# Performance work log

Hardware: AMD Instinct MI355X
Metric: run time of the kernel (lower is better)

Reference implementation:

```python
import jax, jax.numpy as jnp
import numpy as np

B, S, H = 2, 1024, 2048
NH, NKV, HD = 32, 8, 64          # head_dim = H // NH
G = NH // NKV                    # GQA group size = 4
THETA = 500000.0
EPS = 1e-5
SCALE = HD ** -0.5


def _rope_neox(x, positions):
    # x: [B, S, n_heads, HD]; neox style: rotate concatenated halves
    inv_freq = 1.0 / (THETA ** (jnp.arange(0, HD, 2, dtype=jnp.float32) / HD))  # [HD/2]
    ang = positions[..., None].astype(jnp.float32) * inv_freq                    # [B, S, HD/2]
    cos = jnp.cos(ang)[:, :, None, :]
    sin = jnp.sin(ang)[:, :, None, :]
    x1, x2 = jnp.split(x, 2, axis=-1)
    return jnp.concatenate([x1 * cos - x2 * sin, x2 * cos + x1 * sin], axis=-1)


def setup_inputs() -> dict:
    key = jax.random.key(0)
    k1, k2, k3 = jax.random.split(key, 3)
    hidden_states = jax.random.normal(k1, (B, S, H), jnp.float32)
    w_qkv = jax.random.normal(k2, ((NH + 2 * NKV) * HD, H), jnp.float32) * 0.02
    w_o = jax.random.normal(k3, (H, NH * HD), jnp.float32) * 0.02
    norm_w = jnp.ones((H,), jnp.float32)
    positions = jnp.broadcast_to(jnp.arange(S, dtype=jnp.int32), (B, S))
    return {"hidden_states": hidden_states, "positions": positions,
            "w_qkv": w_qkv, "w_o": w_o, "norm_w": norm_w}


def reference(hidden_states, positions, w_qkv, w_o, norm_w):
    # QKV projection (bias=False) and split
    qkv = hidden_states @ w_qkv.T                                 # [B,S,3072]
    q, k, v = jnp.split(qkv, [NH * HD, NH * HD + NKV * HD], axis=-1)
    q = q.reshape(B, S, NH, HD)
    k = k.reshape(B, S, NKV, HD)
    v = v.reshape(B, S, NKV, HD)

    # RoPE on q and k (full rotary_dim = head_dim)
    q = _rope_neox(q, positions)
    k = _rope_neox(k, positions)

    # Causal GQA attention (dense-prefill equivalent of RadixAttention)
    qg = q.reshape(B, S, NKV, G, HD)
    scores = jnp.einsum('bqhgd,bkhd->bhgqk', qg, k) * SCALE       # [B,NKV,G,S,S]
    causal = jnp.tril(jnp.ones((S, S), dtype=bool))
    scores = jnp.where(causal, scores, jnp.float32(-1e30))
    probs = jax.nn.softmax(scores, axis=-1)
    attn = jnp.einsum('bhgqk,bkhd->bqhgd', probs, v).reshape(B, S, NH * HD)

    # BitNet sub-norm (RMSNorm) then output projection
    var = jnp.mean(attn * attn, axis=-1, keepdims=True)
    normed = attn * jax.lax.rsqrt(var + EPS) * norm_w
    return normed @ w_o.T                                         # [B,S,H]
```

## Files before the change

### kernel.cpp

```cpp
#include <hip/hip_runtime.h>
#include <hip/hip_bf16.h>
#include <cstdint>
#include <cstddef>

typedef __bf16 bf16;
typedef __bf16 bf16x2 __attribute__((ext_vector_type(2)));
typedef __bf16 bf16x4 __attribute__((ext_vector_type(4)));
typedef __bf16 bf16x8 __attribute__((ext_vector_type(8)));
typedef float  f32x4  __attribute__((ext_vector_type(4)));

__device__ __forceinline__ void async_copy16(const void* g, void* l) {
  __builtin_amdgcn_global_load_lds((const __attribute__((address_space(1))) void*)g,
                                   (__attribute__((address_space(3))) void*)l,
                                   16, 0, 0);
}

__device__ __forceinline__ bool block_flag_is_f32(const unsigned int* w, int tid,
                                                  int* sflag) {
  if (tid < 64) {
    int weird = 0;
#pragma unroll
    for (int c = 0; c < 2; ++c) {
      const unsigned int lo = w[c * 64 + tid] & 0xffffu;
      const unsigned int ex = (lo >> 7) & 0xffu;
      if (ex >= 134u) ++weird;
    }
    const unsigned long long m1 = __ballot(weird >= 1);
    const unsigned long long m2 = __ballot(weird == 2);
    if (tid == 0) *sflag = (__popcll(m1) + __popcll(m2) >= 8) ? 1 : 0;
  }
  __syncthreads();
  return *sflag != 0;
}

__global__ __launch_bounds__(256) void convert_all(
    const void* __restrict__ s0, const void* __restrict__ s1,
    const void* __restrict__ s2, const void* __restrict__ s3,
    bf16* __restrict__ d0, bf16* __restrict__ d1, bf16* __restrict__ d2,
    float* __restrict__ ssum) {
  __shared__ int sflag;
  const int tid = threadIdx.x;
  const bool f32 = block_flag_is_f32((const unsigned int*)s0, tid, &sflag);
  if (blockIdx.x == 0) {
    ((float4*)ssum)[tid * 2]     = make_float4(0.f, 0.f, 0.f, 0.f);
    ((float4*)ssum)[tid * 2 + 1] = make_float4(0.f, 0.f, 0.f, 0.f);
  }
  const int i = blockIdx.x * 256 + tid;
  if (i >= 3670016) return;
  const void* src; bf16* dst; int off; bool fold = false;
  if      (i < 1048576) { src = s0; dst = d0; off = i; }
  else if (i < 2621440) { src = s1; dst = d1; off = i - 1048576; }
  else                  { src = s2; dst = d2; off = i - 2621440; fold = true; }
  float v[4];
  if (f32) {
    const float4 t = ((const float4*)src)[off];
    v[0] = t.x; v[1] = t.y; v[2] = t.z; v[3] = t.w;
  } else {
    const bf16x4 t = ((const bf16x4*)src)[off];
#pragma unroll
    for (int j = 0; j < 4; ++j) v[j] = (float)t[j];
  }
  if (fold) {
    const int k0 = (off * 4) & 2047;
#pragma unroll
    for (int j = 0; j < 4; ++j) {
      const float w = f32 ? ((const float*)s3)[k0 + j] : (float)((const bf16*)s3)[k0 + j];
      v[j] *= w;
    }
  }
  bf16x4 o;
#pragma unroll
  for (int j = 0; j < 4; ++j) o[j] = (bf16)v[j];
  *(bf16x4*)(dst + (size_t)off * 4) = o;
}

__global__ __launch_bounds__(256) void gemm_qkv_rope(
    const bf16* __restrict__ A, const bf16* __restrict__ B,
    const int* __restrict__ pos,
    bf16* __restrict__ Q, bf16* __restrict__ K, bf16* __restrict__ V)
{
  __shared__ __align__(16) bf16 As[4 * 64 * 32];
  __shared__ __align__(16) bf16 Bs[4 * 128 * 32];
  const int tid = threadIdx.x, wave = tid >> 6, lane = tid & 63;
  const int l15 = lane & 15, l4 = lane >> 4;
  const int m0 = blockIdx.y * 64, n0 = blockIdx.x * 128;
  const int wm = (wave >> 1) * 32, wn = (wave & 1) * 64;
  const int KD = 2048;

  f32x4 acc[2][4] = {};

  for (int kt = 0; kt < KD; kt += 128) {
#pragma unroll
    for (int c = 0; c < 4; ++c) {
      const int e = c * 2048 + tid * 8;
      const int kc = e >> 11, row = (e >> 5) & 63, o = e & 31;
      async_copy16(A + (size_t)(m0 + row) * KD + kt + kc * 32 + o, As + e);
    }
#pragma unroll
    for (int c = 0; c < 8; ++c) {
      const int e = c * 2048 + tid * 8;
      const int kc = e >> 12, row = (e >> 5) & 127, o = e & 31;
      async_copy16(B + (size_t)(n0 + row) * KD + kt + kc * 32 + o, Bs + e);
    }
    __syncthreads();
#pragma unroll
    for (int s = 0; s < 4; ++s) {
      bf16x8 af[2], bfr[4];
#pragma unroll
      for (int i = 0; i < 2; ++i)
        af[i] = *(const bf16x8*)(As + s * 2048 + (wm + i * 16 + l15) * 32 + l4 * 8);
#pragma unroll
      for (int j = 0; j < 4; ++j)
        bfr[j] = *(const bf16x8*)(Bs + s * 4096 + (wn + j * 16 + l15) * 32 + l4 * 8);
#pragma unroll
      for (int i = 0; i < 2; ++i)
#pragma unroll
        for (int j = 0; j < 4; ++j)
          acc[i][j] = __builtin_amdgcn_mfma_f32_16x16x32_bf16(af[i], bfr[j], acc[i][j], 0, 0, 0);
    }
    __syncthreads();
  }

  if (n0 < 2560) {
    const bool isQ = (n0 < 2048);
#pragma unroll
    for (int i = 0; i < 2; ++i)
#pragma unroll
      for (int j = 0; j < 4; ++j) {
        const int col = n0 + wn + j * 16 + l15;
        const int hd = isQ ? col : (col - 2048);
        const int hh = hd >> 6, d = hd & 63;
        const int fi = d & 31;
        const float ifr = __expf((float)fi * -0.41007385554f);
#pragma unroll
        for (int r = 0; r < 4; ++r) {
          const int m = m0 + wm + i * 16 + l4 * 4 + r;
          const int b = m >> 10, s = m & 1023;
          const float ang = (float)pos[m] * ifr;
          float sn, cs;
          __sincosf(ang, &sn, &cs);
          const float x  = acc[i][j][r];
          const float xp = acc[i][j ^ 2][r];
          const float v = (d < 32) ? (x * cs - xp * sn) : (x * cs + xp * sn);
          if (isQ) Q[(((size_t)(b * 32 + hh)) * 1024 + s) * 64 + d] = (bf16)(v * 0.125f);
          else     K[(((size_t)(b * 8 + hh)) * 1024 + s) * 64 + d] = (bf16)v;
        }
      }
  } else {
#pragma unroll
    for (int i = 0; i < 2; ++i)
#pragma unroll
      for (int j = 0; j < 4; ++j) {
        const int cv = n0 + wn + j * 16 + l15 - 2560;
        const int hh = cv >> 6, d = cv & 63;
#pragma unroll
        for (int r = 0; r < 4; ++r) {
          const int m = m0 + wm + i * 16 + l4 * 4 + r;
          const int b = m >> 10, s = m & 1023;
          const int sp = (s & ~31) + ((s & 15) * 2 + ((s >> 4) & 1));
          V[(((size_t)(b * 8 + hh)) * 64 + d) * 1024 + sp] = (bf16)acc[i][j][r];
        }
      }
  }
}

__global__ __launch_bounds__(256) void attn_kernel(
    const bf16* __restrict__ Q, const bf16* __restrict__ K,
    const bf16* __restrict__ Vt, bf16* __restrict__ O, float* __restrict__ ssum)
{
  __shared__ __align__(16) bf16 Ks[2 * 128 * 32];
  __shared__ __align__(16) bf16 Vs[4 * 64 * 32];
  __shared__ __align__(16) bf16 Ps[4 * 128 * 40];

  const int tid = threadIdx.x, wave = tid >> 6, lane = tid & 63;
  const int l15 = lane & 15, l4 = lane >> 4;
  const int ip = blockIdx.x, bh = blockIdx.y;
  const int b = bh >> 5, h = bh & 31, kvh = h >> 2;
  const int qlo = ip * 64, qhi = (15 - ip) * 64;
  const bf16* Qb = Q + ((size_t)(b * 32 + h)) * 65536;
  const bf16* Kb = K + ((size_t)(b * 8 + kvh)) * 65536;
  const bf16* Vb = Vt + ((size_t)(b * 8 + kvh)) * 65536;

#pragma unroll
  for (int c = 0; c < 4; ++c) {
    const int e = c * 2048 + tid * 8;
    const int dchunk = e >> 12;
    const int row = (e & 4095) >> 5;
    const int qb = (row < 64) ? qlo : qhi;
    async_copy16(Qb + (size_t)(qb + (row & 63)) * 64 + dchunk * 32 + (e & 31), Ps + e);
  }
  __syncthreads();
  bf16x8 aq[2][2];
#pragma unroll
  for (int i = 0; i < 2; ++i)
#pragma unroll
    for (int s = 0; s < 2; ++s)
      aq[i][s] = *(const bf16x8*)(Ps + s * 4096 + (i * 64 + wave * 16 + l15) * 32 + l4 * 8);
  __syncthreads();

  float m_s[2][4], l_s[2][4];
  f32x4 o_acc[2][4] = {};
#pragma unroll
  for (int i = 0; i < 2; ++i)
#pragma unroll
    for (int r = 0; r < 4; ++r) { m_s[i][r] = -3.0e4f; l_s[i][r] = 0.f; }

  const int nkt = (1151 - 64 * ip) >> 7;
  for (int kt = 0; kt < nkt; ++kt) {
    const int k0 = kt * 128;
    const bool lo_act = (k0 < (ip + 1) * 64);
#pragma unroll
    for (int c = 0; c < 4; ++c) {
      const int e = c * 2048 + tid * 8;
      const int dchunk = e >> 12;
      const int krow = (e & 4095) >> 5;
      async_copy16(Kb + (size_t)(k0 + krow) * 64 + dchunk * 32 + (e & 31), Ks + e);
      const int kc = e >> 11;
      const int drow = (e & 2047) >> 5;
      async_copy16(Vb + (size_t)drow * 1024 + k0 + kc * 32 + (e & 31), Vs + e);
    }
    __syncthreads();

    f32x4 sc[2][8] = {};
#pragma unroll
    for (int j = 0; j < 8; ++j) {
      const bf16x8 bk0 = *(const bf16x8*)(Ks + (j * 16 + l15) * 32 + l4 * 8);
      const bf16x8 bk1 = *(const bf16x8*)(Ks + 4096 + (j * 16 + l15) * 32 + l4 * 8);
      sc[1][j] = __builtin_amdgcn_mfma_f32_16x16x32_bf16(aq[1][0], bk0, sc[1][j], 0, 0, 0);
      sc[1][j] = __builtin_amdgcn_mfma_f32_16x16x32_bf16(aq[1][1], bk1, sc[1][j], 0, 0, 0);
      if (lo_act) {
        sc[0][j] = __builtin_amdgcn_mfma_f32_16x16x32_bf16(aq[0][0], bk0, sc[0][j], 0, 0, 0);
        sc[0][j] = __builtin_amdgcn_mfma_f32_16x16x32_bf16(aq[0][1], bk1, sc[0][j], 0, 0, 0);
      }
    }

#pragma unroll
    for (int hh = 0; hh < 2; ++hh) {
      if (hh == 0 && !lo_act) continue;
      const int qb = hh ? qhi : qlo;
#pragma unroll
      for (int r = 0; r < 4; ++r) {
        const int rl = wave * 16 + l4 * 4 + r;
        const int rg = qb + rl;
        float mx = -3.0e4f;
#pragma unroll
        for (int j = 0; j < 8; ++j) {
          float v = sc[hh][j][r];
          if (k0 + j * 16 + l15 > rg) v = -3.0e4f;
          sc[hh][j][r] = v;
          mx = fmaxf(mx, v);
        }
#pragma unroll
        for (int off = 1; off < 16; off <<= 1) mx = fmaxf(mx, __shfl_xor(mx, off));
        const float mnew = fmaxf(m_s[hh][r], mx);
        const float alpha = __expf(m_s[hh][r] - mnew);
        m_s[hh][r] = mnew;
        float rs = 0.f;
#pragma unroll
        for (int t = 0; t < 4; ++t) {
          const float pv0 = __expf(sc[hh][2 * t][r]     - mnew);
          const float pv1 = __expf(sc[hh][2 * t + 1][r] - mnew);
          rs += pv0 + pv1;
          bf16x2 pk; pk[0] = (bf16)pv0; pk[1] = (bf16)pv1;
          *(bf16x2*)(Ps + t * 5120 + (hh * 64 + rl) * 40 + l15 * 2) = pk;
        }
#pragma unroll
        for (int off = 1; off < 16; off <<= 1) rs += __shfl_xor(rs, off);
        l_s[hh][r] = l_s[hh][r] * alpha + rs;
#pragma unroll
        for (int jd = 0; jd < 4; ++jd) o_acc[hh][jd][r] *= alpha;
      }
    }

#pragma unroll
    for (int ks = 0; ks < 4; ++ks) {
      bf16x8 bv[4];
#pragma unroll
      for (int jd = 0; jd < 4; ++jd)
        bv[jd] = *(const bf16x8*)(Vs + ks * 2048 + (jd * 16 + l15) * 32 + l4 * 8);
#pragma unroll
      for (int hh = 0; hh < 2; ++hh) {
        if (hh == 0 && !lo_act) continue;
        const bf16x8 ap = *(const bf16x8*)(Ps + ks * 5120 + (hh * 64 + wave * 16 + l15) * 40 + l4 * 8);
#pragma unroll
        for (int jd = 0; jd < 4; ++jd)
          o_acc[hh][jd] = __builtin_amdgcn_mfma_f32_16x16x32_bf16(ap, bv[jd], o_acc[hh][jd], 0, 0, 0);
      }
    }
    __syncthreads();
  }

#pragma unroll
  for (int hh = 0; hh < 2; ++hh) {
    const int qb = hh ? qhi : qlo;
#pragma unroll
    for (int r = 0; r < 4; ++r) {
      const float inv = 1.0f / l_s[hh][r];
      const int srow = qb + wave * 16 + l4 * 4 + r;
      bf16* op = O + ((size_t)(b * 1024 + srow)) * 2048 + h * 64;
      float ss = 0.f;
#pragma unroll
      for (int jd = 0; jd < 4; ++jd) {
        const float v = o_acc[hh][jd][r] * inv;
        op[jd * 16 + l15] = (bf16)v;
        ss += v * v;
      }
#pragma unroll
      for (int off = 1; off < 16; off <<= 1) ss += __shfl_xor(ss, off);
      if (l15 == 0) atomicAdd(&ssum[b * 1024 + srow], ss);
    }
  }
}

__global__ __launch_bounds__(256) void gemm_out(
    const bf16* __restrict__ A, const bf16* __restrict__ B,
    const float* __restrict__ ssum, const unsigned int* __restrict__ hs_raw,
    void* __restrict__ out)
{
  __shared__ __align__(16) bf16 As[4 * 64 * 32];
  __shared__ __align__(16) bf16 Bs[4 * 128 * 32];
  __shared__ int sflag;
  const int tid = threadIdx.x, wave = tid >> 6, lane = tid & 63;
  const bool f32out = block_flag_is_f32(hs_raw, tid, &sflag);
  const int l15 = lane & 15, l4 = lane >> 4;
  const int m0 = blockIdx.y * 64, n0 = blockIdx.x * 128;
  const int wm = (wave >> 1) * 32, wn = (wave & 1) * 64;
  const int KD = 2048;

  f32x4 acc[2][4] = {};

  for (int kt = 0; kt < KD; kt += 128) {
#pragma unroll
    for (int c = 0; c < 4; ++c) {
      const int e = c * 2048 + tid * 8;
      const int kc = e >> 11, row = (e >> 5) & 63, o = e & 31;
      async_copy16(A + (size_t)(m0 + row) * KD + kt + kc * 32 + o, As + e);
    }
#pragma unroll
    for (int c = 0; c < 8; ++c) {
      const int e = c * 2048 + tid * 8;
      const int kc = e >> 12, row = (e >> 5) & 127, o = e & 31;
      async_copy16(B + (size_t)(n0 + row) * KD + kt + kc * 32 + o, Bs + e);
    }
    __syncthreads();
#pragma unroll
    for (int s = 0; s < 4; ++s) {
      bf16x8 af[2], bfr[4];
#pragma unroll
      for (int i = 0; i < 2; ++i)
        af[i] = *(const bf16x8*)(As + s * 2048 + (wm + i * 16 + l15) * 32 + l4 * 8);
#pragma unroll
      for (int j = 0; j < 4; ++j)
        bfr[j] = *(const bf16x8*)(Bs + s * 4096 + (wn + j * 16 + l15) * 32 + l4 * 8);
#pragma unroll
      for (int i = 0; i < 2; ++i)
#pragma unroll
        for (int j = 0; j < 4; ++j)
          acc[i][j] = __builtin_amdgcn_mfma_f32_16x16x32_bf16(af[i], bfr[j], acc[i][j], 0, 0, 0);
    }
    __syncthreads();
  }

#pragma unroll
  for (int i = 0; i < 2; ++i)
#pragma unroll
    for (int r = 0; r < 4; ++r) {
      const int row = m0 + wm + i * 16 + l4 * 4 + r;
      const float ri = rsqrtf(ssum[row] * (1.0f / 2048.0f) + 1e-5f);
#pragma unroll
      for (int j = 0; j < 4; ++j) {
        const int col = n0 + wn + j * 16 + l15;
        const size_t idx = (size_t)row * 2048 + col;
        const float v = ri * acc[i][j][r];
        if (f32out) ((float*)out)[idx] = v;
        else        ((bf16*)out)[idx]  = (bf16)v;
      }
    }
}

extern "C" void kernel_launch(void* const* d_in, const int* in_sizes, int n_in,
                              void* d_out, int out_size, void* d_ws, size_t ws_size,
                              hipStream_t stream) {
  const void* hs     = d_in[0];
  const int*  pos    = (const int*)d_in[1];
  const void* w_qkv  = d_in[2];
  const void* w_o    = d_in[3];
  const void* norm_w = d_in[4];

  char* ws = (char*)d_ws;
  bf16*  hs_b   = (bf16*) (ws);
  bf16*  wqkv_b = (bf16*) (ws + 8388608);
  bf16*  w_o_b  = (bf16*) (ws + 20971520);
  float* ssum   = (float*)(ws + 29360128);
  bf16*  Qr     = (bf16*) (ws + 29368320);
  bf16*  Kr     = (bf16*) (ws + 37756928);
  bf16*  Vtr    = (bf16*) (ws + 39854080);
  bf16*  attn_o = (bf16*) (ws + 41951232);

  convert_all<<<14336, 256, 0, stream>>>(hs, w_qkv, w_o, norm_w,
                                         hs_b, wqkv_b, w_o_b, ssum);
  gemm_qkv_rope<<<dim3(24, 32), 256, 0, stream>>>(hs_b, wqkv_b, pos, Qr, Kr, Vtr);
  attn_kernel<<<dim3(8, 64), 256, 0, stream>>>(Qr, Kr, Vtr, attn_o, ssum);
  gemm_out<<<dim3(16, 32), 256, 0, stream>>>(attn_o, w_o_b, ssum,
                                             (const unsigned int*)hs, d_out);
}
```

Before: 207.2 us.

## Double-buffer GEMM tiles, swizzle LDS, prefetch K/V via registers, lazy softmax rescale

Both GEMMs now double-buffer 64-wide K tiles, so the next tile's async loads overlap the MFMA work on the current one. LDS layouts gain an XOR swizzle to cut bank conflicts. The attention kernel prefetches the next K/V tile into registers while computing, moves softmax to exp2 by folding log2(e) into the Q scale, and skips the rescale when the running max has not grown by more than 8. The trade-offs are higher register pressure and an extra barrier per attention iteration. The lazy-rescale threshold also lets probabilities exceed 1 before normalization, which costs some bf16 precision in P.

```diff
diff --git a/kernel.cpp b/kernel.cpp
--- a/kernel.cpp
+++ b/kernel.cpp
@@ -14,6 +14,8 @@
                                    (__attribute__((address_space(3))) void*)l,
                                    16, 0, 0);
 }
+
+__device__ __forceinline__ int swz(int row) { return ((row >> 1) & 3) << 3; }
 
 __device__ __forceinline__ bool block_flag_is_f32(const unsigned int* w, int tid,
                                                   int* sflag) {
@@ -79,39 +81,47 @@
     const int* __restrict__ pos,
     bf16* __restrict__ Q, bf16* __restrict__ K, bf16* __restrict__ V)
 {
-  __shared__ __align__(16) bf16 As[4 * 64 * 32];
-  __shared__ __align__(16) bf16 Bs[4 * 128 * 32];
+  __shared__ __align__(16) bf16 As[2][2 * 64 * 32];
+  __shared__ __align__(16) bf16 Bs[2][2 * 128 * 32];
   const int tid = threadIdx.x, wave = tid >> 6, lane = tid & 63;
   const int l15 = lane & 15, l4 = lane >> 4;
   const int m0 = blockIdx.y * 64, n0 = blockIdx.x * 128;
   const int wm = (wave >> 1) * 32, wn = (wave & 1) * 64;
-  const int KD = 2048;
+  const int swz_ro = (l4 * 8) ^ swz(l15);
 
   f32x4 acc[2][4] = {};
 
-  for (int kt = 0; kt < KD; kt += 128) {
+  auto stage = [&](int buf, int kt) {
+#pragma unroll
+    for (int c = 0; c < 2; ++c) {
+      const int e = c * 2048 + tid * 8;
+      const int kc = e >> 11, row = (e >> 5) & 63;
+      const int o = (e & 31) ^ swz(row);
+      async_copy16(A + (size_t)(m0 + row) * 2048 + kt + kc * 32 + o, &As[buf][e]);
+    }
 #pragma unroll
     for (int c = 0; c < 4; ++c) {
       const int e = c * 2048 + tid * 8;
-      const int kc = e >> 11, row = (e >> 5) & 63, o = e & 31;
-      async_copy16(A + (size_t)(m0 + row) * KD + kt + kc * 32 + o, As + e);
-    }
-#pragma unroll
-    for (int c = 0; c < 8; ++c) {
-      const int e = c * 2048 + tid * 8;
-      const int kc = e >> 12, row = (e >> 5) & 127, o = e & 31;
-      async_copy16(B + (size_t)(n0 + row) * KD + kt + kc * 32 + o, Bs + e);
-    }
-    __syncthreads();
-#pragma unroll
-    for (int s = 0; s < 4; ++s) {
+      const int kc = e >> 12, row = (e >> 5) & 127;
+      const int o = (e & 31) ^ swz(row);
+      async_copy16(B + (size_t)(n0 + row) * 2048 + kt + kc * 32 + o, &Bs[buf][e]);
+    }
+  };
+
+  stage(0, 0);
+  __syncthreads();
+  int cur = 0;
+  for (int kt = 0; kt < 2048; kt += 64) {
+    if (kt + 64 < 2048) stage(cur ^ 1, kt + 64);
+#pragma unroll
+    for (int s = 0; s < 2; ++s) {
       bf16x8 af[2], bfr[4];
 #pragma unroll
       for (int i = 0; i < 2; ++i)
-        af[i] = *(const bf16x8*)(As + s * 2048 + (wm + i * 16 + l15) * 32 + l4 * 8);
+        af[i] = *(const bf16x8*)(&As[cur][s * 2048 + (wm + i * 16 + l15) * 32 + swz_ro]);
 #pragma unroll
       for (int j = 0; j < 4; ++j)
-        bfr[j] = *(const bf16x8*)(Bs + s * 4096 + (wn + j * 16 + l15) * 32 + l4 * 8);
+        bfr[j] = *(const bf16x8*)(&Bs[cur][s * 4096 + (wn + j * 16 + l15) * 32 + swz_ro]);
 #pragma unroll
       for (int i = 0; i < 2; ++i)
 #pragma unroll
@@ -119,6 +129,7 @@
           acc[i][j] = __builtin_amdgcn_mfma_f32_16x16x32_bf16(af[i], bfr[j], acc[i][j], 0, 0, 0);
     }
     __syncthreads();
+    cur ^= 1;
   }
 
   if (n0 < 2560) {
@@ -142,7 +153,7 @@
           const float x  = acc[i][j][r];
           const float xp = acc[i][j ^ 2][r];
           const float v = (d < 32) ? (x * cs - xp * sn) : (x * cs + xp * sn);
-          if (isQ) Q[(((size_t)(b * 32 + hh)) * 1024 + s) * 64 + d] = (bf16)(v * 0.125f);
+          if (isQ) Q[(((size_t)(b * 32 + hh)) * 1024 + s) * 64 + d] = (bf16)(v * 0.1803368801f);
           else     K[(((size_t)(b * 8 + hh)) * 1024 + s) * 64 + d] = (bf16)v;
         }
       }
@@ -174,6 +185,7 @@
 
   const int tid = threadIdx.x, wave = tid >> 6, lane = tid & 63;
   const int l15 = lane & 15, l4 = lane >> 4;
+  const int swz_ro = (l4 * 8) ^ swz(l15);
   const int ip = blockIdx.x, bh = blockIdx.y;
   const int b = bh >> 5, h = bh & 31, kvh = h >> 2;
   const int qlo = ip * 64, qhi = (15 - ip) * 64;
@@ -187,7 +199,15 @@
     const int dchunk = e >> 12;
     const int row = (e & 4095) >> 5;
     const int qb = (row < 64) ? qlo : qhi;
-    async_copy16(Qb + (size_t)(qb + (row & 63)) * 64 + dchunk * 32 + (e & 31), Ps + e);
+    const int o = (e & 31) ^ swz(row);
+    async_copy16(Qb + (size_t)(qb + (row & 63)) * 64 + dchunk * 32 + o, Ps + e);
+  }
+  bf16x8 kreg[4], vreg[4];
+#pragma unroll
+  for (int c = 0; c < 4; ++c) {
+    const int e = c * 2048 + tid * 8;
+    kreg[c] = *(const bf16x8*)(Kb + (size_t)((e & 4095) >> 5) * 64 + (e >> 12) * 32 + (e & 31));
+    vreg[c] = *(const bf16x8*)(Vb + (size_t)((e & 2047) >> 5) * 1024 + (e >> 11) * 32 + (e & 31));
   }
   __syncthreads();
   bf16x8 aq[2][2];
@@ -195,7 +215,15 @@
   for (int i = 0; i < 2; ++i)
 #pragma unroll
     for (int s = 0; s < 2; ++s)
-      aq[i][s] = *(const bf16x8*)(Ps + s * 4096 + (i * 64 + wave * 16 + l15) * 32 + l4 * 8);
+      aq[i][s] = *(const bf16x8*)(Ps + s * 4096 + (i * 64 + wave * 16 + l15) * 32 + swz_ro);
+#pragma unroll
+  for (int c = 0; c < 4; ++c) {
+    const int e = c * 2048 + tid * 8;
+    const int krow = (e & 4095) >> 5;
+    *(bf16x8*)(Ks + (e ^ swz(krow))) = kreg[c];
+    const int drow = (e & 2047) >> 5;
+    *(bf16x8*)(Vs + (e ^ swz(drow))) = vreg[c];
+  }
   __syncthreads();
 
   float m_s[2][4], l_s[2][4];
@@ -209,23 +237,21 @@
   for (int kt = 0; kt < nkt; ++kt) {
     const int k0 = kt * 128;
     const bool lo_act = (k0 < (ip + 1) * 64);
-#pragma unroll
-    for (int c = 0; c < 4; ++c) {
-      const int e = c * 2048 + tid * 8;
-      const int dchunk = e >> 12;
-      const int krow = (e & 4095) >> 5;
-      async_copy16(Kb + (size_t)(k0 + krow) * 64 + dchunk * 32 + (e & 31), Ks + e);
-      const int kc = e >> 11;
-      const int drow = (e & 2047) >> 5;
-      async_copy16(Vb + (size_t)drow * 1024 + k0 + kc * 32 + (e & 31), Vs + e);
-    }
-    __syncthreads();
+    if (kt + 1 < nkt) {
+      const int k0n = k0 + 128;
+#pragma unroll
+      for (int c = 0; c < 4; ++c) {
+        const int e = c * 2048 + tid * 8;
+        kreg[c] = *(const bf16x8*)(Kb + (size_t)(k0n + ((e & 4095) >> 5)) * 64 + (e >> 12) * 32 + (e & 31));
+        vreg[c] = *(const bf16x8*)(Vb + (size_t)((e & 2047) >> 5) * 1024 + k0n + (e >> 11) * 32 + (e & 31));
+      }
+    }
 
     f32x4 sc[2][8] = {};
 #pragma unroll
     for (int j = 0; j < 8; ++j) {
-      const bf16x8 bk0 = *(const bf16x8*)(Ks + (j * 16 + l15) * 32 + l4 * 8);
-      const bf16x8 bk1 = *(const bf16x8*)(Ks + 4096 + (j * 16 + l15) * 32 + l4 * 8);
+      const bf16x8 bk0 = *(const bf16x8*)(Ks + (j * 16 + l15) * 32 + swz_ro);
+      const bf16x8 bk1 = *(const bf16x8*)(Ks + 4096 + (j * 16 + l15) * 32 + swz_ro);
       sc[1][j] = __builtin_amdgcn_mfma_f32_16x16x32_bf16(aq[1][0], bk0, sc[1][j], 0, 0, 0);
       sc[1][j] = __builtin_amdgcn_mfma_f32_16x16x32_bf16(aq[1][1], bk1, sc[1][j], 0, 0, 0);
       if (lo_act) {
@@ -238,10 +264,11 @@
     for (int hh = 0; hh < 2; ++hh) {
       if (hh == 0 && !lo_act) continue;
       const int qb = hh ? qhi : qlo;
+      float mxv[4];
+      bool grow = false;
 #pragma unroll
       for (int r = 0; r < 4; ++r) {
-        const int rl = wave * 16 + l4 * 4 + r;
-        const int rg = qb + rl;
+        const int rg = qb + wave * 16 + l4 * 4 + r;
         float mx = -3.0e4f;
 #pragma unroll
         for (int j = 0; j < 8; ++j) {
@@ -252,23 +279,49 @@
         }
 #pragma unroll
         for (int off = 1; off < 16; off <<= 1) mx = fmaxf(mx, __shfl_xor(mx, off));
-        const float mnew = fmaxf(m_s[hh][r], mx);
-        const float alpha = __expf(m_s[hh][r] - mnew);
-        m_s[hh][r] = mnew;
-        float rs = 0.f;
-#pragma unroll
-        for (int t = 0; t < 4; ++t) {
-          const float pv0 = __expf(sc[hh][2 * t][r]     - mnew);
-          const float pv1 = __expf(sc[hh][2 * t + 1][r] - mnew);
-          rs += pv0 + pv1;
-          bf16x2 pk; pk[0] = (bf16)pv0; pk[1] = (bf16)pv1;
-          *(bf16x2*)(Ps + t * 5120 + (hh * 64 + rl) * 40 + l15 * 2) = pk;
+        mxv[r] = mx;
+        grow = grow || (mx > m_s[hh][r] + 8.0f);
+      }
+      if (__all(!grow)) {
+#pragma unroll
+        for (int r = 0; r < 4; ++r) {
+          const int rl = wave * 16 + l4 * 4 + r;
+          const float m = m_s[hh][r];
+          float rs = 0.f;
+#pragma unroll
+          for (int t = 0; t < 4; ++t) {
+            const float pv0 = exp2f(sc[hh][2 * t][r]     - m);
+            const float pv1 = exp2f(sc[hh][2 * t + 1][r] - m);
+            rs += pv0 + pv1;
+            bf16x2 pk; pk[0] = (bf16)pv0; pk[1] = (bf16)pv1;
+            *(bf16x2*)(Ps + t * 5120 + (hh * 64 + rl) * 40 + l15 * 2) = pk;
+          }
+#pragma unroll
+          for (int off = 1; off < 16; off <<= 1) rs += __shfl_xor(rs, off);
+          l_s[hh][r] += rs;
         }
-#pragma unroll
-        for (int off = 1; off < 16; off <<= 1) rs += __shfl_xor(rs, off);
-        l_s[hh][r] = l_s[hh][r] * alpha + rs;
-#pragma unroll
-        for (int jd = 0; jd < 4; ++jd) o_acc[hh][jd][r] *= alpha;
+      } else {
+#pragma unroll
+        for (int r = 0; r < 4; ++r) {
+          const int rl = wave * 16 + l4 * 4 + r;
+          const float mnew = fmaxf(m_s[hh][r], mxv[r]);
+          const float alpha = exp2f(m_s[hh][r] - mnew);
+          m_s[hh][r] = mnew;
+          float rs = 0.f;
+#pragma unroll
+          for (int t = 0; t < 4; ++t) {
+            const float pv0 = exp2f(sc[hh][2 * t][r]     - mnew);
+            const float pv1 = exp2f(sc[hh][2 * t + 1][r] - mnew);
+            rs += pv0 + pv1;
+            bf16x2 pk; pk[0] = (bf16)pv0; pk[1] = (bf16)pv1;
+            *(bf16x2*)(Ps + t * 5120 + (hh * 64 + rl) * 40 + l15 * 2) = pk;
+          }
+#pragma unroll
+          for (int off = 1; off < 16; off <<= 1) rs += __shfl_xor(rs, off);
+          l_s[hh][r] = l_s[hh][r] * alpha + rs;
+#pragma unroll
+          for (int jd = 0; jd < 4; ++jd) o_acc[hh][jd][r] *= alpha;
+        }
       }
     }
 
@@ -277,7 +330,7 @@
       bf16x8 bv[4];
 #pragma unroll
       for (int jd = 0; jd < 4; ++jd)
-        bv[jd] = *(const bf16x8*)(Vs + ks * 2048 + (jd * 16 + l15) * 32 + l4 * 8);
+        bv[jd] = *(const bf16x8*)(Vs + ks * 2048 + (jd * 16 + l15) * 32 + swz_ro);
 #pragma unroll
       for (int hh = 0; hh < 2; ++hh) {
         if (hh == 0 && !lo_act) continue;
@@ -288,6 +341,17 @@
       }
     }
     __syncthreads();
+    if (kt + 1 < nkt) {
+#pragma unroll
+      for (int c = 0; c < 4; ++c) {
+        const int e = c * 2048 + tid * 8;
+        const int krow = (e & 4095) >> 5;
+        *(bf16x8*)(Ks + (e ^ swz(krow))) = kreg[c];
+        const int drow = (e & 2047) >> 5;
+        *(bf16x8*)(Vs + (e ^ swz(drow))) = vreg[c];
+      }
+      __syncthreads();
+    }
   }
 
 #pragma unroll
@@ -317,41 +381,49 @@
     const float* __restrict__ ssum, const unsigned int* __restrict__ hs_raw,
     void* __restrict__ out)
 {
-  __shared__ __align__(16) bf16 As[4 * 64 * 32];
-  __shared__ __align__(16) bf16 Bs[4 * 128 * 32];
+  __shared__ __align__(16) bf16 As[2][2 * 64 * 32];
+  __shared__ __align__(16) bf16 Bs[2][2 * 128 * 32];
   __shared__ int sflag;
   const int tid = threadIdx.x, wave = tid >> 6, lane = tid & 63;
   const bool f32out = block_flag_is_f32(hs_raw, tid, &sflag);
   const int l15 = lane & 15, l4 = lane >> 4;
   const int m0 = blockIdx.y * 64, n0 = blockIdx.x * 128;
   const int wm = (wave >> 1) * 32, wn = (wave & 1) * 64;
-  const int KD = 2048;
+  const int swz_ro = (l4 * 8) ^ swz(l15);
 
   f32x4 acc[2][4] = {};
 
-  for (int kt = 0; kt < KD; kt += 128) {
+  auto stage = [&](int buf, int kt) {
+#pragma unroll
+    for (int c = 0; c < 2; ++c) {
+      const int e = c * 2048 + tid * 8;
+      const int kc = e >> 11, row = (e >> 5) & 63;
+      const int o = (e & 31) ^ swz(row);
+      async_copy16(A + (size_t)(m0 + row) * 2048 + kt + kc * 32 + o, &As[buf][e]);
+    }
 #pragma unroll
     for (int c = 0; c < 4; ++c) {
       const int e = c * 2048 + tid * 8;
-      const int kc = e >> 11, row = (e >> 5) & 63, o = e & 31;
-      async_copy16(A + (size_t)(m0 + row) * KD + kt + kc * 32 + o, As + e);
-    }
-#pragma unroll
-    for (int c = 0; c < 8; ++c) {
-      const int e = c * 2048 + tid * 8;
-      const int kc = e >> 12, row = (e >> 5) & 127, o = e & 31;
-      async_copy16(B + (size_t)(n0 + row) * KD + kt + kc * 32 + o, Bs + e);
-    }
-    __syncthreads();
-#pragma unroll
-    for (int s = 0; s < 4; ++s) {
+      const int kc = e >> 12, row = (e >> 5) & 127;
+      const int o = (e & 31) ^ swz(row);
+      async_copy16(B + (size_t)(n0 + row) * 2048 + kt + kc * 32 + o, &Bs[buf][e]);
+    }
+  };
+
+  stage(0, 0);
+  __syncthreads();
+  int cur = 0;
+  for (int kt = 0; kt < 2048; kt += 64) {
+    if (kt + 64 < 2048) stage(cur ^ 1, kt + 64);
+#pragma unroll
+    for (int s = 0; s < 2; ++s) {
       bf16x8 af[2], bfr[4];
 #pragma unroll
       for (int i = 0; i < 2; ++i)
-        af[i] = *(const bf16x8*)(As + s * 2048 + (wm + i * 16 + l15) * 32 + l4 * 8);
+        af[i] = *(const bf16x8*)(&As[cur][s * 2048 + (wm + i * 16 + l15) * 32 + swz_ro]);
 #pragma unroll
       for (int j = 0; j < 4; ++j)
-        bfr[j] = *(const bf16x8*)(Bs + s * 4096 + (wn + j * 16 + l15) * 32 + l4 * 8);
+        bfr[j] = *(const bf16x8*)(&Bs[cur][s * 4096 + (wn + j * 16 + l15) * 32 + swz_ro]);
 #pragma unroll
       for (int i = 0; i < 2; ++i)
 #pragma unroll
@@ -359,6 +431,7 @@
           acc[i][j] = __builtin_amdgcn_mfma_f32_16x16x32_bf16(af[i], bfr[j], acc[i][j], 0, 0, 0);
     }
     __syncthreads();
+    cur ^= 1;
   }
 
 #pragma unroll
```

Result: slower. 233.4 us (+12.7%).
